# Performance work log

Measured on AMD Instinct MI355X. Metric: run time of the kernel, lower is better.

## Reference

```python
import jax, jax.numpy as jnp
import numpy as np

N = 100000
E = 1600000
F_IN = 64
F_OUT = 64
C = 1.0
MIN_NORM = 1e-15
BALL_EPS = 4e-3  # float32 eps in HGCN PoincareBall.proj


def _norm(x):
    return jnp.clip(jnp.linalg.norm(x, axis=-1, keepdims=True), MIN_NORM)


def artanh(x):
    return jnp.arctanh(jnp.clip(x, -1.0 + 1e-7, 1.0 - 1e-7))


def proj(x, c):
    # project back onto the Poincare ball of curvature -c
    norm = _norm(x)
    maxnorm = (1.0 - BALL_EPS) / jnp.sqrt(c)
    return jnp.where(norm > maxnorm, x / norm * maxnorm, x)


def mobius_matvec(m, x, c):
    sqrt_c = jnp.sqrt(c)
    x_norm = _norm(x)
    mx = x @ m.T
    mx_norm = _norm(mx)
    res = jnp.tanh(mx_norm / x_norm * artanh(sqrt_c * x_norm)) * mx / (mx_norm * sqrt_c)
    zero_mx = jnp.all(mx == 0, axis=-1, keepdims=True)
    return jnp.where(zero_mx, jnp.zeros_like(res), res)


def expmap0(u, c):
    sqrt_c = jnp.sqrt(c)
    u_norm = _norm(u)
    return jnp.tanh(sqrt_c * u_norm) * u / (sqrt_c * u_norm)


def mobius_add(x, y, c):
    x2 = jnp.sum(x * x, axis=-1, keepdims=True)
    y2 = jnp.sum(y * y, axis=-1, keepdims=True)
    xy = jnp.sum(x * y, axis=-1, keepdims=True)
    num = (1.0 + 2.0 * c * xy + c * y2) * x + (1.0 - c * x2) * y
    denom = 1.0 + 2.0 * c * xy + c * c * x2 * y2
    return num / jnp.clip(denom, MIN_NORM)


def hyp_linear(x, W, b, c):
    res = proj(mobius_matvec(W, x, c), c)
    if b is not None:
        hyp_bias = proj(expmap0(b[None, :], c), c)
        res = proj(mobius_add(res, hyp_bias, c), c)
    return res


def scatter_mean(edge_index, x, n):
    # mean of source features over edges landing at each target node; 0 if isolated
    src, dst = edge_index[0], edge_index[1]
    s = jax.ops.segment_sum(x[src], dst, num_segments=n)
    cnt = jax.ops.segment_sum(jnp.ones((src.shape[0], 1), x.dtype), dst, num_segments=n)
    return s / jnp.clip(cnt, 1.0)


def setup_inputs() -> dict:
    key = jax.random.key(0)
    ks = jax.random.split(key, 9)
    glorot = 1.0 / np.sqrt(F_IN)
    return {
        "x": jax.random.normal(ks[0], (N, F_IN), dtype=jnp.float32) * 0.1,
        "W_pos": jax.random.uniform(ks[1], (F_OUT, F_IN), jnp.float32, -glorot, glorot),
        "W_pos_cc": jax.random.uniform(ks[2], (F_OUT, F_IN), jnp.float32, -glorot, glorot),
        "b_pos_cc": jax.random.uniform(ks[3], (F_OUT,), jnp.float32, -glorot, glorot),
        "W_neg": jax.random.uniform(ks[4], (F_OUT, F_IN), jnp.float32, -glorot, glorot),
        "W_neg_cc": jax.random.uniform(ks[5], (F_OUT, F_IN), jnp.float32, -glorot, glorot),
        "b_neg_cc": jax.random.uniform(ks[6], (F_OUT,), jnp.float32, -glorot, glorot),
        "pos_edge_index": jax.random.randint(ks[7], (2, E), 0, N, dtype=jnp.int64) if jax.config.jax_enable_x64 else jax.random.randint(ks[7], (2, E), 0, N, dtype=jnp.int32),
        "neg_edge_index": jax.random.randint(ks[8], (2, E), 0, N, dtype=jnp.int32),
    }


def reference(x, W_pos, W_pos_cc, b_pos_cc, W_neg, W_neg_cc, b_neg_cc, pos_edge_index, neg_edge_index):
    n = x.shape[0]
    # first_aggr=True branch of HSignedConv.forward
    agg_pos = scatter_mean(pos_edge_index, x, n)          # [N, F_IN]
    out_pos = hyp_linear(agg_pos, W_pos, None, C)
    out_pos = out_pos + hyp_linear(x, W_pos_cc, b_pos_cc, C)
    agg_neg = scatter_mean(neg_edge_index, x, n)
    out_neg = hyp_linear(agg_neg, W_neg, None, C)
    out_neg = out_neg + hyp_linear(x, W_neg_cc, b_neg_cc, C)
    return jnp.concatenate([out_pos, out_neg], axis=-1)  # [N, 2*F_OUT]
```

## Files before the change

kernel.cpp:

```cpp
#include <hip/hip_runtime.h>
#include <math.h>

#define NN 100000
#define BSZ 256
#define NB 391
#define NB2 782
constexpr float MAXNORM_C = 0.996f;
constexpr float MINNORM_C = 1e-15f;

__global__ void prep_transpose(const float* __restrict__ Wp, const float* __restrict__ Wpc,
                               const float* __restrict__ Wn, const float* __restrict__ Wnc,
                               float* __restrict__ wt) {
    int idx = blockIdx.x * 256 + threadIdx.x;
    int m = idx >> 12;
    int k = (idx >> 6) & 63;
    int j = idx & 63;
    const float* W = (m == 0) ? Wp : (m == 1) ? Wpc : (m == 2) ? Wn : Wnc;
    wt[idx] = W[j * 64 + k];
}

__device__ inline float wave_sum64(float v) {
    #pragma unroll
    for (int m = 32; m >= 1; m >>= 1) v += __shfl_xor(v, m, 64);
    return v;
}

__global__ void prep_bias(const float* __restrict__ bp, const float* __restrict__ bn,
                          float* __restrict__ hb) {
    int l = threadIdx.x;
    #pragma unroll
    for (int h = 0; h < 2; ++h) {
        float u = (h ? bn : bp)[l];
        float norm = fmaxf(sqrtf(wave_sum64(u * u)), MINNORM_C);
        float s = tanhf(norm) / norm;
        float v = s * u;
        float vn = fmaxf(sqrtf(wave_sum64(v * v)), MINNORM_C);
        if (vn > MAXNORM_C) v *= MAXNORM_C / vn;
        float y2 = wave_sum64(v * v);
        hb[h * 65 + l] = v;
        if (l == 0) hb[h * 65 + 64] = y2;
    }
}

__global__ __launch_bounds__(256) void bucket_count(
    const int* __restrict__ pei, int E1,
    const int* __restrict__ nei, int E2,
    int* __restrict__ gcnt) {
    __shared__ int h[NB2];
    int tid = threadIdx.x;
    for (int i = tid; i < NB2; i += 256) h[i] = 0;
    __syncthreads();
    int tot = E1 + E2;
    int base = blockIdx.x * 8192;
    #pragma unroll 4
    for (int k = 0; k < 32; ++k) {
        int idx = base + k * 256 + tid;
        if (idx < tot) {
            int half = idx >= E1;
            int e = idx - (half ? E1 : 0);
            const int* ei = half ? nei : pei;
            int E = half ? E2 : E1;
            int dst = ei[E + e];
            atomicAdd(&h[half * NB + (dst >> 8)], 1);
        }
    }
    __syncthreads();
    for (int i = tid; i < NB2; i += 256) {
        int c = h[i];
        if (c) atomicAdd(&gcnt[i], c);
    }
}

__global__ void bucket_scan(const int* __restrict__ gcnt, int* __restrict__ goffs,
                            int* __restrict__ gcursor) {
    __shared__ int tmp[256];
    int tid = threadIdx.x;
    int base = tid * 4;
    int items[4];
    int s = 0;
    #pragma unroll
    for (int i = 0; i < 4; ++i) {
        items[i] = (base + i < NB2) ? gcnt[base + i] : 0;
        s += items[i];
    }
    tmp[tid] = s;
    __syncthreads();
    for (int off = 1; off < 256; off <<= 1) {
        int v = (tid >= off) ? tmp[tid - off] : 0;
        __syncthreads();
        tmp[tid] += v;
        __syncthreads();
    }
    int run = tmp[tid] - s;
    #pragma unroll
    for (int i = 0; i < 4; ++i) {
        if (base + i < NB2) { goffs[base + i] = run; gcursor[base + i] = run; }
        run += items[i];
    }
}

__global__ __launch_bounds__(256) void bucket_scatter(
    const int* __restrict__ pei, int E1,
    const int* __restrict__ nei, int E2,
    int* __restrict__ gcursor, int* __restrict__ packed) {
    __shared__ int h[NB2];
    __shared__ int hb[NB2];
    int tid = threadIdx.x;
    for (int i = tid; i < NB2; i += 256) h[i] = 0;
    __syncthreads();
    int tot = E1 + E2;
    int base = blockIdx.x * 8192;
    #pragma unroll 4
    for (int k = 0; k < 32; ++k) {
        int idx = base + k * 256 + tid;
        if (idx < tot) {
            int half = idx >= E1;
            int e = idx - (half ? E1 : 0);
            const int* ei = half ? nei : pei;
            int E = half ? E2 : E1;
            int dst = ei[E + e];
            atomicAdd(&h[half * NB + (dst >> 8)], 1);
        }
    }
    __syncthreads();
    for (int i = tid; i < NB2; i += 256) {
        int c = h[i];
        hb[i] = c ? atomicAdd(&gcursor[i], c) : 0;
    }
    __syncthreads();
    for (int i = tid; i < NB2; i += 256) h[i] = 0;
    __syncthreads();
    #pragma unroll 4
    for (int k = 0; k < 32; ++k) {
        int idx = base + k * 256 + tid;
        if (idx < tot) {
            int half = idx >= E1;
            int e = idx - (half ? E1 : 0);
            const int* ei = half ? nei : pei;
            int E = half ? E2 : E1;
            int src = ei[e];
            int dst = ei[E + e];
            int b = half * NB + (dst >> 8);
            int r = atomicAdd(&h[b], 1);
            packed[hb[b] + r] = (src << 8) | (dst & 255);
        }
    }
}

__global__ __launch_bounds__(256) void node_sort(
    const int* __restrict__ goffs, const int* __restrict__ gcnt,
    const int* __restrict__ packed,
    int* __restrict__ esrc, int* __restrict__ ndeg, int* __restrict__ noffs) {
    __shared__ int h[256];
    __shared__ int sc[256];
    int tid = threadIdx.x;
    int bucket = blockIdx.x;
    int start = goffs[bucket];
    int cnt = gcnt[bucket];
    h[tid] = 0;
    __syncthreads();
    for (int i = start + tid; i < start + cnt; i += 256)
        atomicAdd(&h[packed[i] & 255], 1);
    __syncthreads();
    int deg = h[tid];
    sc[tid] = deg;
    __syncthreads();
    for (int off = 1; off < 256; off <<= 1) {
        int v = (tid >= off) ? sc[tid - off] : 0;
        __syncthreads();
        sc[tid] += v;
        __syncthreads();
    }
    int excl = sc[tid] - deg;
    int half = bucket >= NB;
    int node = (bucket - (half ? NB : 0)) * BSZ + tid;
    if (node < NN) {
        ndeg[half * NN + node] = deg;
        noffs[half * NN + node] = start + excl;
    }
    h[tid] = excl;
    __syncthreads();
    for (int i = start + tid; i < start + cnt; i += 256) {
        int p = packed[i];
        int r = atomicAdd(&h[p & 255], 1);
        esrc[start + r] = p >> 8;
    }
}

__global__ __launch_bounds__(256) void gather_kernel(
    const int* __restrict__ noffs, const int* __restrict__ ndeg,
    const int* __restrict__ esrc, const float* __restrict__ x,
    float* __restrict__ out) {
    int wid = (blockIdx.x * 256 + threadIdx.x) >> 6;
    int lane = threadIdx.x & 63;
    if (wid >= 2 * NN) return;
    int half = wid >= NN;
    int node = wid - (half ? NN : 0);
    int start = noffs[wid];
    int deg = ndeg[wid];
    float acc = 0.f;
    for (int b = 0; b < deg; b += 64) {
        int n = min(64, deg - b);
        int s_l = (b + lane < deg) ? esrc[start + b + lane] : 0;
        int i = 0;
        for (; i + 4 <= n; i += 4) {
            int a0 = __shfl(s_l, i, 64), a1 = __shfl(s_l, i + 1, 64);
            int a2 = __shfl(s_l, i + 2, 64), a3 = __shfl(s_l, i + 3, 64);
            float v0 = x[a0 * 64 + lane], v1 = x[a1 * 64 + lane];
            float v2 = x[a2 * 64 + lane], v3 = x[a3 * 64 + lane];
            acc += (v0 + v1) + (v2 + v3);
        }
        for (; i < n; ++i) acc += x[__shfl(s_l, i, 64) * 64 + lane];
    }
    float m = acc / fmaxf((float)deg, 1.f);
    out[(size_t)node * 128 + half * 64 + lane] = m;
}

__device__ inline void hyp_mm_proj(const float* vp, float cinv,
                                   const float* __restrict__ wtm, float (&mx)[64]) {
    #pragma unroll
    for (int j = 0; j < 64; ++j) mx[j] = 0.f;
    float vn2 = 0.f;
    for (int k0 = 0; k0 < 64; k0 += 4) {
        float4 a4 = *(const float4*)(vp + k0);
        float a0 = a4.x * cinv, a1 = a4.y * cinv, a2 = a4.z * cinv, a3 = a4.w * cinv;
        vn2 = fmaf(a0, a0, fmaf(a1, a1, fmaf(a2, a2, fmaf(a3, a3, vn2))));
        const float* w0 = wtm + k0 * 64;
        #pragma unroll
        for (int j = 0; j < 64; ++j) {
            float m = mx[j];
            m = fmaf(a0, w0[j],        m);
            m = fmaf(a1, w0[64 + j],   m);
            m = fmaf(a2, w0[128 + j],  m);
            m = fmaf(a3, w0[192 + j],  m);
            mx[j] = m;
        }
    }
    float mn2 = 0.f;
    #pragma unroll
    for (int j = 0; j < 64; ++j) mn2 = fmaf(mx[j], mx[j], mn2);
    float xnorm = fmaxf(sqrtf(vn2), MINNORM_C);
    float mnorm = fmaxf(sqrtf(mn2), MINNORM_C);
    float z = fminf(xnorm, 1.0f - 1e-7f);
    float art = 0.5f * logf((1.0f + z) / (1.0f - z));
    float t = tanhf(mnorm / xnorm * art);
    float scale = (mn2 == 0.f) ? 0.f : (t / mnorm);
    #pragma unroll
    for (int j = 0; j < 64; ++j) mx[j] *= scale;
    float rn2 = 0.f;
    #pragma unroll
    for (int j = 0; j < 64; ++j) rn2 = fmaf(mx[j], mx[j], rn2);
    float rnorm = fmaxf(sqrtf(rn2), MINNORM_C);
    float f = (rnorm > MAXNORM_C) ? (MAXNORM_C / rnorm) : 1.0f;
    #pragma unroll
    for (int j = 0; j < 64; ++j) mx[j] *= f;
}

__global__ __launch_bounds__(256, 2) void finalize_kernel(
    const float* __restrict__ x,
    const float* __restrict__ wt,
    const float* __restrict__ hb,
    float* __restrict__ out) {
    int half = blockIdx.x & 1;
    int group = (blockIdx.x >> 1) * 4 + (threadIdx.x >> 6);
    int lane = threadIdx.x & 63;
    int node = group * 64 + lane;
    bool valid = node < NN;
    int nc = valid ? node : NN - 1;
    float* op = out + (size_t)nc * 128 + half * 64;

    const float* wtA = wt + half * 8192;
    const float* wtB = wtA + 4096;
    const float* hbh = hb + half * 65;

    {
        float resA[64];
        hyp_mm_proj(op, 1.0f, wtA, resA);
        if (valid) {
            #pragma unroll
            for (int k0 = 0; k0 < 64; k0 += 4)
                *(float4*)(op + k0) = make_float4(resA[k0], resA[k0+1], resA[k0+2], resA[k0+3]);
        }
    }

    float resB[64];
    hyp_mm_proj(x + (size_t)nc * 64, 1.0f, wtB, resB);

    float x2 = 0.f, xy = 0.f;
    #pragma unroll
    for (int j = 0; j < 64; ++j) {
        x2 = fmaf(resB[j], resB[j], x2);
        xy = fmaf(resB[j], hbh[j], xy);
    }
    float y2 = hbh[64];
    float A = 1.f + 2.f * xy + y2;
    float B = 1.f - x2;
    float den = 1.f + 2.f * xy + x2 * y2;
    float dinv = 1.f / fmaxf(den, MINNORM_C);
    float rn2 = 0.f;
    #pragma unroll
    for (int j = 0; j < 64; ++j) {
        float r = (A * resB[j] + B * hbh[j]) * dinv;
        resB[j] = r;
        rn2 = fmaf(r, r, rn2);
    }
    float rnorm = fmaxf(sqrtf(rn2), MINNORM_C);
    float f = (rnorm > MAXNORM_C) ? (MAXNORM_C / rnorm) : 1.0f;

    if (valid) {
        #pragma unroll
        for (int k0 = 0; k0 < 64; k0 += 4) {
            float4 a = *(const float4*)(op + k0);
            a.x += resB[k0 + 0] * f;
            a.y += resB[k0 + 1] * f;
            a.z += resB[k0 + 2] * f;
            a.w += resB[k0 + 3] * f;
            *(float4*)(op + k0) = a;
        }
    }
}

extern "C" void kernel_launch(void* const* d_in, const int* in_sizes, int n_in,
                              void* d_out, int out_size, void* d_ws, size_t ws_size,
                              hipStream_t stream) {
    const float* x   = (const float*)d_in[0];
    const float* Wp  = (const float*)d_in[1];
    const float* Wpc = (const float*)d_in[2];
    const float* bp  = (const float*)d_in[3];
    const float* Wn  = (const float*)d_in[4];
    const float* Wnc = (const float*)d_in[5];
    const float* bn  = (const float*)d_in[6];
    const int* pei = (const int*)d_in[7];
    const int* nei = (const int*)d_in[8];
    float* out = (float*)d_out;

    int E1 = in_sizes[7] / 2;
    int E2 = in_sizes[8] / 2;
    int tot = E1 + E2;

    int*   gcnt    = (int*)d_ws;
    int*   goffs   = gcnt + NB2;
    int*   gcursor = goffs + NB2;
    int*   ndeg    = gcursor + NB2 + 2;
    int*   noffs   = ndeg + 2 * NN;
    float* hbp     = (float*)(noffs + 2 * NN);
    float* wt      = hbp + 192;
    int*   packed  = (int*)(wt + 16384);
    int*   esrc    = packed + tot;

    hipMemsetAsync(gcnt, 0, NB2 * sizeof(int), stream);

    prep_transpose<<<64, 256, 0, stream>>>(Wp, Wpc, Wn, Wnc, wt);
    prep_bias<<<1, 64, 0, stream>>>(bp, bn, hbp);

    int nblk = (tot + 8191) / 8192;
    bucket_count<<<nblk, 256, 0, stream>>>(pei, E1, nei, E2, gcnt);
    bucket_scan<<<1, 256, 0, stream>>>(gcnt, goffs, gcursor);
    bucket_scatter<<<nblk, 256, 0, stream>>>(pei, E1, nei, E2, gcursor, packed);
    node_sort<<<NB2, 256, 0, stream>>>(goffs, gcnt, packed, esrc, ndeg, noffs);

    gather_kernel<<<(2 * NN * 64 + 255) / 256, 256, 0, stream>>>(noffs, ndeg, esrc, x, out);

    int groups = (NN + 63) / 64;
    int blocks = 2 * ((groups + 3) / 4);
    finalize_kernel<<<blocks, 256, 0, stream>>>(x, wt, hbp, out);
}
```

Before: 421.1 us.

## Stage weights in LDS and compute two nodes per thread in finalize

The finalize kernel now copies each half's transposed weight matrices into shared memory. Each thread processes two nodes at once, so every weight float4 loaded from LDS feeds two rows of FMAs. Block size drops to 128 threads covering 256 nodes, and the k-loop is kept rolled. The aim is to cut global/L1 weight traffic and raise the FMA-to-load ratio, at the cost of much higher register pressure (two 64-float accumulators per thread) and possible spills or lower occupancy.

```diff
diff --git a/kernel.cpp b/kernel.cpp
--- a/kernel.cpp
+++ b/kernel.cpp
@@ -216,29 +216,44 @@
     out[(size_t)node * 128 + half * 64 + lane] = m;
 }
 
-__device__ inline void hyp_mm_proj(const float* vp, float cinv,
-                                   const float* __restrict__ wtm, float (&mx)[64]) {
-    #pragma unroll
-    for (int j = 0; j < 64; ++j) mx[j] = 0.f;
-    float vn2 = 0.f;
+__device__ __attribute__((always_inline)) inline void mm2(
+        const float* p1, const float* p2, const float4* wl,
+        float (&m1)[64], float (&m2)[64], float& vo1, float& vo2) {
+    #pragma unroll
+    for (int j = 0; j < 64; ++j) { m1[j] = 0.f; m2[j] = 0.f; }
+    float v1 = 0.f, v2 = 0.f;
+    #pragma unroll 1
     for (int k0 = 0; k0 < 64; k0 += 4) {
-        float4 a4 = *(const float4*)(vp + k0);
-        float a0 = a4.x * cinv, a1 = a4.y * cinv, a2 = a4.z * cinv, a3 = a4.w * cinv;
-        vn2 = fmaf(a0, a0, fmaf(a1, a1, fmaf(a2, a2, fmaf(a3, a3, vn2))));
-        const float* w0 = wtm + k0 * 64;
+        float4 a = *(const float4*)(p1 + k0);
+        float4 b = *(const float4*)(p2 + k0);
+        v1 = fmaf(a.x, a.x, fmaf(a.y, a.y, fmaf(a.z, a.z, fmaf(a.w, a.w, v1))));
+        v2 = fmaf(b.x, b.x, fmaf(b.y, b.y, fmaf(b.z, b.z, fmaf(b.w, b.w, v2))));
+        const float4* wk = wl + k0 * 16;
         #pragma unroll
-        for (int j = 0; j < 64; ++j) {
-            float m = mx[j];
-            m = fmaf(a0, w0[j],        m);
-            m = fmaf(a1, w0[64 + j],   m);
-            m = fmaf(a2, w0[128 + j],  m);
-            m = fmaf(a3, w0[192 + j],  m);
-            mx[j] = m;
-        }
-    }
+        for (int j4 = 0; j4 < 16; ++j4) {
+            float4 w0 = wk[j4];
+            float4 w1 = wk[16 + j4];
+            float4 w2 = wk[32 + j4];
+            float4 w3 = wk[48 + j4];
+            int j = j4 * 4;
+            m1[j+0] = fmaf(a.x,w0.x, fmaf(a.y,w1.x, fmaf(a.z,w2.x, fmaf(a.w,w3.x, m1[j+0]))));
+            m1[j+1] = fmaf(a.x,w0.y, fmaf(a.y,w1.y, fmaf(a.z,w2.y, fmaf(a.w,w3.y, m1[j+1]))));
+            m1[j+2] = fmaf(a.x,w0.z, fmaf(a.y,w1.z, fmaf(a.z,w2.z, fmaf(a.w,w3.z, m1[j+2]))));
+            m1[j+3] = fmaf(a.x,w0.w, fmaf(a.y,w1.w, fmaf(a.z,w2.w, fmaf(a.w,w3.w, m1[j+3]))));
+            m2[j+0] = fmaf(b.x,w0.x, fmaf(b.y,w1.x, fmaf(b.z,w2.x, fmaf(b.w,w3.x, m2[j+0]))));
+            m2[j+1] = fmaf(b.x,w0.y, fmaf(b.y,w1.y, fmaf(b.z,w2.y, fmaf(b.w,w3.y, m2[j+1]))));
+            m2[j+2] = fmaf(b.x,w0.z, fmaf(b.y,w1.z, fmaf(b.z,w2.z, fmaf(b.w,w3.z, m2[j+2]))));
+            m2[j+3] = fmaf(b.x,w0.w, fmaf(b.y,w1.w, fmaf(b.z,w2.w, fmaf(b.w,w3.w, m2[j+3]))));
+        }
+    }
+    vo1 = v1; vo2 = v2;
+}
+
+__device__ __attribute__((always_inline)) inline void mob_scale_proj(
+        float (&m)[64], float vn2) {
     float mn2 = 0.f;
     #pragma unroll
-    for (int j = 0; j < 64; ++j) mn2 = fmaf(mx[j], mx[j], mn2);
+    for (int j = 0; j < 64; ++j) mn2 = fmaf(m[j], m[j], mn2);
     float xnorm = fmaxf(sqrtf(vn2), MINNORM_C);
     float mnorm = fmaxf(sqrtf(mn2), MINNORM_C);
     float z = fminf(xnorm, 1.0f - 1e-7f);
@@ -246,53 +261,26 @@
     float t = tanhf(mnorm / xnorm * art);
     float scale = (mn2 == 0.f) ? 0.f : (t / mnorm);
     #pragma unroll
-    for (int j = 0; j < 64; ++j) mx[j] *= scale;
+    for (int j = 0; j < 64; ++j) m[j] *= scale;
     float rn2 = 0.f;
     #pragma unroll
-    for (int j = 0; j < 64; ++j) rn2 = fmaf(mx[j], mx[j], rn2);
+    for (int j = 0; j < 64; ++j) rn2 = fmaf(m[j], m[j], rn2);
     float rnorm = fmaxf(sqrtf(rn2), MINNORM_C);
     float f = (rnorm > MAXNORM_C) ? (MAXNORM_C / rnorm) : 1.0f;
     #pragma unroll
-    for (int j = 0; j < 64; ++j) mx[j] *= f;
-}
-
-__global__ __launch_bounds__(256, 2) void finalize_kernel(
-    const float* __restrict__ x,
-    const float* __restrict__ wt,
-    const float* __restrict__ hb,
-    float* __restrict__ out) {
-    int half = blockIdx.x & 1;
-    int group = (blockIdx.x >> 1) * 4 + (threadIdx.x >> 6);
-    int lane = threadIdx.x & 63;
-    int node = group * 64 + lane;
-    bool valid = node < NN;
-    int nc = valid ? node : NN - 1;
-    float* op = out + (size_t)nc * 128 + half * 64;
-
-    const float* wtA = wt + half * 8192;
-    const float* wtB = wtA + 4096;
-    const float* hbh = hb + half * 65;
-
-    {
-        float resA[64];
-        hyp_mm_proj(op, 1.0f, wtA, resA);
-        if (valid) {
-            #pragma unroll
-            for (int k0 = 0; k0 < 64; k0 += 4)
-                *(float4*)(op + k0) = make_float4(resA[k0], resA[k0+1], resA[k0+2], resA[k0+3]);
-        }
-    }
-
-    float resB[64];
-    hyp_mm_proj(x + (size_t)nc * 64, 1.0f, wtB, resB);
-
+    for (int j = 0; j < 64; ++j) m[j] *= f;
+}
+
+__device__ __attribute__((always_inline)) inline float bias_addf(
+        float (&m)[64], const float* hbv) {
     float x2 = 0.f, xy = 0.f;
     #pragma unroll
     for (int j = 0; j < 64; ++j) {
-        x2 = fmaf(resB[j], resB[j], x2);
-        xy = fmaf(resB[j], hbh[j], xy);
-    }
-    float y2 = hbh[64];
+        float h = hbv[j];
+        x2 = fmaf(m[j], m[j], x2);
+        xy = fmaf(m[j], h, xy);
+    }
+    float y2 = hbv[64];
     float A = 1.f + 2.f * xy + y2;
     float B = 1.f - x2;
     float den = 1.f + 2.f * xy + x2 * y2;
@@ -300,22 +288,88 @@
     float rn2 = 0.f;
     #pragma unroll
     for (int j = 0; j < 64; ++j) {
-        float r = (A * resB[j] + B * hbh[j]) * dinv;
-        resB[j] = r;
+        float r = (A * m[j] + B * hbv[j]) * dinv;
+        m[j] = r;
         rn2 = fmaf(r, r, rn2);
     }
     float rnorm = fmaxf(sqrtf(rn2), MINNORM_C);
-    float f = (rnorm > MAXNORM_C) ? (MAXNORM_C / rnorm) : 1.0f;
-
-    if (valid) {
-        #pragma unroll
-        for (int k0 = 0; k0 < 64; k0 += 4) {
-            float4 a = *(const float4*)(op + k0);
-            a.x += resB[k0 + 0] * f;
-            a.y += resB[k0 + 1] * f;
-            a.z += resB[k0 + 2] * f;
-            a.w += resB[k0 + 3] * f;
-            *(float4*)(op + k0) = a;
+    return (rnorm > MAXNORM_C) ? (MAXNORM_C / rnorm) : 1.0f;
+}
+
+__global__ __launch_bounds__(128, 2) void finalize_kernel(
+    const float* __restrict__ x,
+    const float* __restrict__ wt,
+    const float* __restrict__ hb,
+    float* __restrict__ out) {
+    __shared__ float4 wlds[2048];
+    __shared__ __align__(16) float hbs[68];
+    int tid = threadIdx.x;
+    int half = blockIdx.x & 1;
+    int base = (blockIdx.x >> 1) * 256;
+
+    const float4* wsrc = (const float4*)(wt + half * 8192);
+    #pragma unroll
+    for (int i = 0; i < 16; ++i) wlds[i * 128 + tid] = wsrc[i * 128 + tid];
+    if (tid < 65) hbs[tid] = hb[half * 65 + tid];
+    __syncthreads();
+
+    int lane = tid & 63;
+    int wave = tid >> 6;
+    int n1 = base + wave * 128 + lane;
+    int n2 = n1 + 64;
+    bool v1 = n1 < NN, v2 = n2 < NN;
+    int c1 = v1 ? n1 : NN - 1, c2 = v2 ? n2 : NN - 1;
+    float* op1 = out + (size_t)c1 * 128 + half * 64;
+    float* op2 = out + (size_t)c2 * 128 + half * 64;
+
+    {
+        float m1[64], m2[64];
+        float vnA1, vnA2;
+        mm2(op1, op2, wlds, m1, m2, vnA1, vnA2);
+        mob_scale_proj(m1, vnA1);
+        mob_scale_proj(m2, vnA2);
+        if (v1) {
+            #pragma unroll
+            for (int k0 = 0; k0 < 64; k0 += 4)
+                *(float4*)(op1 + k0) = make_float4(m1[k0], m1[k0+1], m1[k0+2], m1[k0+3]);
+        }
+        if (v2) {
+            #pragma unroll
+            for (int k0 = 0; k0 < 64; k0 += 4)
+                *(float4*)(op2 + k0) = make_float4(m2[k0], m2[k0+1], m2[k0+2], m2[k0+3]);
+        }
+    }
+
+    {
+        float m1[64], m2[64];
+        float vnB1, vnB2;
+        mm2(x + (size_t)c1 * 64, x + (size_t)c2 * 64, wlds + 1024, m1, m2, vnB1, vnB2);
+        mob_scale_proj(m1, vnB1);
+        mob_scale_proj(m2, vnB2);
+        float f1 = bias_addf(m1, hbs);
+        float f2 = bias_addf(m2, hbs);
+
+        if (v1) {
+            #pragma unroll
+            for (int k0 = 0; k0 < 64; k0 += 4) {
+                float4 a = *(const float4*)(op1 + k0);
+                a.x += m1[k0 + 0] * f1;
+                a.y += m1[k0 + 1] * f1;
+                a.z += m1[k0 + 2] * f1;
+                a.w += m1[k0 + 3] * f1;
+                *(float4*)(op1 + k0) = a;
+            }
+        }
+        if (v2) {
+            #pragma unroll
+            for (int k0 = 0; k0 < 64; k0 += 4) {
+                float4 a = *(const float4*)(op2 + k0);
+                a.x += m2[k0 + 0] * f2;
+                a.y += m2[k0 + 1] * f2;
+                a.z += m2[k0 + 2] * f2;
+                a.w += m2[k0 + 3] * f2;
+                *(float4*)(op2 + k0) = a;
+            }
         }
     }
 }
@@ -361,7 +415,6 @@
 
     gather_kernel<<<(2 * NN * 64 + 255) / 256, 256, 0, stream>>>(noffs, ndeg, esrc, x, out);
 
-    int groups = (NN + 63) / 64;
-    int blocks = 2 * ((groups + 3) / 4);
-    finalize_kernel<<<blocks, 256, 0, stream>>>(x, wt, hbp, out);
-}
+    int fblocks = 2 * ((NN + 255) / 256);
+    finalize_kernel<<<fblocks, 128, 0, stream>>>(x, wt, hbp, out);
+}
```

New measurement: 414.7 us. No clear change (-1.5%).

## Rewrite finalize as wave-per-node with register-resident weights and DPP reductions

Applied to the files above, without the earlier changes.

The finalize kernel changes from one node per thread, with a 64-wide accumulator array and weight reads from a transposed buffer, to one node per wavefront with one output feature per lane. Each lane keeps its row of both weight matrices in registers and broadcasts input features with readlane. Norms are reduced with DPP and a final readlane, and a persistent grid-stride loop over 768 blocks replaces the per-node grid. This drops the transpose prep kernel, lets each lane do coalesced loads and stores of a single float, and removes the heavy per-thread register arrays, at the cost of 64 serial readlane+FMA steps per matvec and several cross-lane reductions per node.

```diff
diff --git a/kernel.cpp b/kernel.cpp
--- a/kernel.cpp
+++ b/kernel.cpp
@@ -5,19 +5,9 @@
 #define BSZ 256
 #define NB 391
 #define NB2 782
+#define FW 1536
 constexpr float MAXNORM_C = 0.996f;
 constexpr float MINNORM_C = 1e-15f;
-
-__global__ void prep_transpose(const float* __restrict__ Wp, const float* __restrict__ Wpc,
-                               const float* __restrict__ Wn, const float* __restrict__ Wnc,
-                               float* __restrict__ wt) {
-    int idx = blockIdx.x * 256 + threadIdx.x;
-    int m = idx >> 12;
-    int k = (idx >> 6) & 63;
-    int j = idx & 63;
-    const float* W = (m == 0) ? Wp : (m == 1) ? Wpc : (m == 2) ? Wn : Wnc;
-    wt[idx] = W[j * 64 + k];
-}
 
 __device__ inline float wave_sum64(float v) {
     #pragma unroll
@@ -216,107 +206,96 @@
     out[(size_t)node * 128 + half * 64 + lane] = m;
 }
 
-__device__ inline void hyp_mm_proj(const float* vp, float cinv,
-                                   const float* __restrict__ wtm, float (&mx)[64]) {
-    #pragma unroll
-    for (int j = 0; j < 64; ++j) mx[j] = 0.f;
-    float vn2 = 0.f;
-    for (int k0 = 0; k0 < 64; k0 += 4) {
-        float4 a4 = *(const float4*)(vp + k0);
-        float a0 = a4.x * cinv, a1 = a4.y * cinv, a2 = a4.z * cinv, a3 = a4.w * cinv;
-        vn2 = fmaf(a0, a0, fmaf(a1, a1, fmaf(a2, a2, fmaf(a3, a3, vn2))));
-        const float* w0 = wtm + k0 * 64;
-        #pragma unroll
-        for (int j = 0; j < 64; ++j) {
-            float m = mx[j];
-            m = fmaf(a0, w0[j],        m);
-            m = fmaf(a1, w0[64 + j],   m);
-            m = fmaf(a2, w0[128 + j],  m);
-            m = fmaf(a3, w0[192 + j],  m);
-            mx[j] = m;
-        }
-    }
-    float mn2 = 0.f;
-    #pragma unroll
-    for (int j = 0; j < 64; ++j) mn2 = fmaf(mx[j], mx[j], mn2);
-    float xnorm = fmaxf(sqrtf(vn2), MINNORM_C);
-    float mnorm = fmaxf(sqrtf(mn2), MINNORM_C);
-    float z = fminf(xnorm, 1.0f - 1e-7f);
-    float art = 0.5f * logf((1.0f + z) / (1.0f - z));
-    float t = tanhf(mnorm / xnorm * art);
-    float scale = (mn2 == 0.f) ? 0.f : (t / mnorm);
-    #pragma unroll
-    for (int j = 0; j < 64; ++j) mx[j] *= scale;
-    float rn2 = 0.f;
-    #pragma unroll
-    for (int j = 0; j < 64; ++j) rn2 = fmaf(mx[j], mx[j], rn2);
-    float rnorm = fmaxf(sqrtf(rn2), MINNORM_C);
-    float f = (rnorm > MAXNORM_C) ? (MAXNORM_C / rnorm) : 1.0f;
-    #pragma unroll
-    for (int j = 0; j < 64; ++j) mx[j] *= f;
+__device__ __forceinline__ float dpp_sum_bcast(float x) {
+    x += __int_as_float(__builtin_amdgcn_update_dpp(0, __float_as_int(x), 0x111, 0xf, 0xf, true));
+    x += __int_as_float(__builtin_amdgcn_update_dpp(0, __float_as_int(x), 0x112, 0xf, 0xf, true));
+    x += __int_as_float(__builtin_amdgcn_update_dpp(0, __float_as_int(x), 0x114, 0xf, 0xf, true));
+    x += __int_as_float(__builtin_amdgcn_update_dpp(0, __float_as_int(x), 0x118, 0xf, 0xf, true));
+    x += __int_as_float(__builtin_amdgcn_update_dpp(0, __float_as_int(x), 0x142, 0xa, 0xf, true));
+    x += __int_as_float(__builtin_amdgcn_update_dpp(0, __float_as_int(x), 0x143, 0xc, 0xf, true));
+    return __int_as_float(__builtin_amdgcn_readlane(__float_as_int(x), 63));
+}
+
+__device__ __forceinline__ float readlane_f(float v, int l) {
+    return __int_as_float(__builtin_amdgcn_readlane(__float_as_int(v), l));
 }
 
 __global__ __launch_bounds__(256, 2) void finalize_kernel(
     const float* __restrict__ x,
-    const float* __restrict__ wt,
+    const float* __restrict__ Wp, const float* __restrict__ Wpc,
+    const float* __restrict__ Wn, const float* __restrict__ Wnc,
     const float* __restrict__ hb,
-    float* __restrict__ out) {
+    float* out) {
+    int tid = threadIdx.x;
+    int lane = tid & 63;
+    int wslot = __builtin_amdgcn_readfirstlane(tid >> 6);
     int half = blockIdx.x & 1;
-    int group = (blockIdx.x >> 1) * 4 + (threadIdx.x >> 6);
-    int lane = threadIdx.x & 63;
-    int node = group * 64 + lane;
-    bool valid = node < NN;
-    int nc = valid ? node : NN - 1;
-    float* op = out + (size_t)nc * 128 + half * 64;
-
-    const float* wtA = wt + half * 8192;
-    const float* wtB = wtA + 4096;
-    const float* hbh = hb + half * 65;
-
-    {
-        float resA[64];
-        hyp_mm_proj(op, 1.0f, wtA, resA);
-        if (valid) {
-            #pragma unroll
-            for (int k0 = 0; k0 < 64; k0 += 4)
-                *(float4*)(op + k0) = make_float4(resA[k0], resA[k0+1], resA[k0+2], resA[k0+3]);
-        }
-    }
-
-    float resB[64];
-    hyp_mm_proj(x + (size_t)nc * 64, 1.0f, wtB, resB);
-
-    float x2 = 0.f, xy = 0.f;
-    #pragma unroll
-    for (int j = 0; j < 64; ++j) {
-        x2 = fmaf(resB[j], resB[j], x2);
-        xy = fmaf(resB[j], hbh[j], xy);
-    }
-    float y2 = hbh[64];
-    float A = 1.f + 2.f * xy + y2;
-    float B = 1.f - x2;
-    float den = 1.f + 2.f * xy + x2 * y2;
-    float dinv = 1.f / fmaxf(den, MINNORM_C);
-    float rn2 = 0.f;
-    #pragma unroll
-    for (int j = 0; j < 64; ++j) {
-        float r = (A * resB[j] + B * hbh[j]) * dinv;
-        resB[j] = r;
-        rn2 = fmaf(r, r, rn2);
-    }
-    float rnorm = fmaxf(sqrtf(rn2), MINNORM_C);
-    float f = (rnorm > MAXNORM_C) ? (MAXNORM_C / rnorm) : 1.0f;
-
-    if (valid) {
+    int widx = (blockIdx.x >> 1) * 4 + wslot;
+
+    const float* WA = half ? Wn : Wp;
+    const float* WB = half ? Wnc : Wpc;
+    float wA[64], wB[64];
+    #pragma unroll
+    for (int k4 = 0; k4 < 16; ++k4) {
+        float4 t = *(const float4*)(WA + lane * 64 + k4 * 4);
+        wA[k4*4+0] = t.x; wA[k4*4+1] = t.y; wA[k4*4+2] = t.z; wA[k4*4+3] = t.w;
+        float4 u = *(const float4*)(WB + lane * 64 + k4 * 4);
+        wB[k4*4+0] = u.x; wB[k4*4+1] = u.y; wB[k4*4+2] = u.z; wB[k4*4+3] = u.w;
+    }
+    float hbv = hb[half * 65 + lane];
+    float y2s = hb[half * 65 + 64];
+
+    for (int node = widx; node < NN; node += FW) {
+        size_t obase = (size_t)node * 128 + half * 64;
+
+        float av = out[obase + lane];
+        float vn2 = dpp_sum_bcast(av * av);
+        float m = 0.f;
         #pragma unroll
-        for (int k0 = 0; k0 < 64; k0 += 4) {
-            float4 a = *(const float4*)(op + k0);
-            a.x += resB[k0 + 0] * f;
-            a.y += resB[k0 + 1] * f;
-            a.z += resB[k0 + 2] * f;
-            a.w += resB[k0 + 3] * f;
-            *(float4*)(op + k0) = a;
-        }
+        for (int k = 0; k < 64; ++k)
+            m = fmaf(readlane_f(av, k), wA[k], m);
+        float mn2 = dpp_sum_bcast(m * m);
+        float xnorm = fmaxf(sqrtf(vn2), MINNORM_C);
+        float mnorm = fmaxf(sqrtf(mn2), MINNORM_C);
+        float z = fminf(xnorm, 1.0f - 1e-7f);
+        float art = 0.5f * logf((1.0f + z) / (1.0f - z));
+        float t = tanhf(mnorm / xnorm * art);
+        float scale = (mn2 == 0.f) ? 0.f : (t / mnorm);
+        float resA = m * scale;
+        float rn2 = mn2 * scale * scale;
+        float rn = fmaxf(sqrtf(rn2), MINNORM_C);
+        if (rn > MAXNORM_C) resA *= MAXNORM_C / rn;
+
+        float xv = x[(size_t)node * 64 + lane];
+        float vn2b = dpp_sum_bcast(xv * xv);
+        float mB = 0.f;
+        #pragma unroll
+        for (int k = 0; k < 64; ++k)
+            mB = fmaf(readlane_f(xv, k), wB[k], mB);
+        float mn2b = dpp_sum_bcast(mB * mB);
+        float xnb = fmaxf(sqrtf(vn2b), MINNORM_C);
+        float mnb = fmaxf(sqrtf(mn2b), MINNORM_C);
+        float zb = fminf(xnb, 1.0f - 1e-7f);
+        float artb = 0.5f * logf((1.0f + zb) / (1.0f - zb));
+        float tb = tanhf(mnb / xnb * artb);
+        float scb = (mn2b == 0.f) ? 0.f : (tb / mnb);
+        float pB = mB * scb;
+        float pn2 = mn2b * scb * scb;
+        float prn = fmaxf(sqrtf(pn2), MINNORM_C);
+        float fp = (prn > MAXNORM_C) ? (MAXNORM_C / prn) : 1.0f;
+        pB *= fp;
+        float x2 = pn2 * fp * fp;
+        float xy = dpp_sum_bcast(pB * hbv);
+        float A = 1.f + 2.f * xy + y2s;
+        float Bc = 1.f - x2;
+        float den = 1.f + 2.f * xy + x2 * y2s;
+        float dinv = 1.f / fmaxf(den, MINNORM_C);
+        float r = (A * pB + Bc * hbv) * dinv;
+        float rn2c = dpp_sum_bcast(r * r);
+        float rnc = fmaxf(sqrtf(rn2c), MINNORM_C);
+        float f2 = (rnc > MAXNORM_C) ? (MAXNORM_C / rnc) : 1.0f;
+
+        out[obase + lane] = resA + r * f2;
     }
 }
 
@@ -344,13 +323,11 @@
     int*   ndeg    = gcursor + NB2 + 2;
     int*   noffs   = ndeg + 2 * NN;
     float* hbp     = (float*)(noffs + 2 * NN);
-    float* wt      = hbp + 192;
-    int*   packed  = (int*)(wt + 16384);
+    int*   packed  = (int*)(hbp + 192);
     int*   esrc    = packed + tot;
 
     hipMemsetAsync(gcnt, 0, NB2 * sizeof(int), stream);
 
-    prep_transpose<<<64, 256, 0, stream>>>(Wp, Wpc, Wn, Wnc, wt);
     prep_bias<<<1, 64, 0, stream>>>(bp, bn, hbp);
 
     int nblk = (tot + 8191) / 8192;
@@ -361,7 +338,5 @@
 
     gather_kernel<<<(2 * NN * 64 + 255) / 256, 256, 0, stream>>>(noffs, ndeg, esrc, x, out);
 
-    int groups = (NN + 63) / 64;
-    int blocks = 2 * ((groups + 3) / 4);
-    finalize_kernel<<<blocks, 256, 0, stream>>>(x, wt, hbp, out);
-}
+    finalize_kernel<<<768, 256, 0, stream>>>(x, Wp, Wpc, Wn, Wnc, hbp, out);
+}
```

Result: slower. 564.3 us (+34.0%).
